# Optimization experiments

Hardware: AMD Instinct MI355X
Metric: run time of the kernel (lower is better)

The kernel has to match this reference:

```python
import jax, jax.numpy as jnp
import numpy as np

GRID_SIZE = 5
SPLINE_ORDER = 3
GRID_RANGE = (-1.0, 1.0)


def b_splines(x, grid, spline_order=SPLINE_ORDER):
    # x: [B, in], grid: [G] with G = grid_size + 2*spline_order + 1
    x = x[..., None]                      # [B, in, 1]
    g = grid[None, None, :]               # [1, 1, G]
    bases = ((x >= g[..., :-1]) & (x < g[..., 1:])).astype(x.dtype)  # [B, in, G-1]
    for k in range(1, spline_order + 1):
        left = (x - g[..., :-(k + 1)]) / (g[..., k:-1] - g[..., :-(k + 1)]) * bases[..., :-1]
        right = (g[..., k + 1:] - x) / (g[..., k + 1:] - g[..., 1:-k]) * bases[..., 1:]
        bases = left + right
    return bases                          # [B, in, grid_size + spline_order]


def setup_inputs() -> dict:
    key = jax.random.key(0)
    k1, k2, k3, k4 = jax.random.split(key, 4)
    B, IN, OUT = 32768, 256, 256
    n_coef = GRID_SIZE + SPLINE_ORDER  # 8
    h = (GRID_RANGE[1] - GRID_RANGE[0]) / GRID_SIZE
    grid = jnp.arange(-SPLINE_ORDER, GRID_SIZE + SPLINE_ORDER + 1, dtype=jnp.float32) * h + GRID_RANGE[0]  # [12]
    x = jax.random.normal(k1, (B, IN), dtype=jnp.float32)
    base_weight = jax.random.normal(k2, (OUT, IN), dtype=jnp.float32) * np.sqrt(2.0 / IN)
    spline_weight = jax.random.normal(k3, (OUT, IN, n_coef), dtype=jnp.float32) * (0.1 / GRID_SIZE)
    spline_scaler = jax.random.normal(k4, (OUT, IN), dtype=jnp.float32) * np.sqrt(2.0 / IN)
    return {"x": x, "base_weight": base_weight, "spline_weight": spline_weight,
            "spline_scaler": spline_scaler, "grid": grid}


def reference(x, base_weight, spline_weight, spline_scaler, grid):
    B = x.shape[0]
    out_features = base_weight.shape[0]
    # base branch: silu(x) @ base_weight^T
    base_out = jnp.matmul(jax.nn.silu(x), base_weight.T)  # [B, out]
    # spline branch
    bases = b_splines(x, grid)                             # [B, in, n_coef]
    scaled_w = spline_weight * spline_scaler[..., None]    # [out, in, n_coef]
    spline_out = jnp.matmul(bases.reshape(B, -1), scaled_w.reshape(out_features, -1).T)
    return base_out + spline_out
```

## Files before the change

kernel.cpp:

```cpp
#include <hip/hip_runtime.h>
#include <hip/hip_bf16.h>
#include <stdint.h>


#define IN_F 256
#define OUT_F 256
#define KDIM 2304
#define BK 64
#define NCHUNK (KDIM / BK)
#define TBINS 512
#define WC_BYTES ((size_t)OUT_F * KDIM * 2)

#define AS1 __attribute__((address_space(1)))
#define AS3 __attribute__((address_space(3)))

typedef float f32x4 __attribute__((ext_vector_type(4)));
typedef short bf16x8 __attribute__((ext_vector_type(8)));

__device__ __forceinline__ uint32_t f2bf(float f) {
    union { float f; uint32_t u; } c; c.f = f;
    uint32_t u = c.u;
    return (u + 0x7FFFu + ((u >> 16) & 1u)) >> 16;
}

__device__ __forceinline__ float silu_f(float v) {
    return v / (1.0f + __expf(-v));
}

__global__ void build_w(const float* __restrict__ bw, const float* __restrict__ sw,
                        const float* __restrict__ ss, unsigned short* __restrict__ Wc,
                        uint64_t* __restrict__ tg) {
    const int o = blockIdx.x;
    const int i = threadIdx.x;
    Wc[o * KDIM + i] = (unsigned short)f2bf(bw[o * IN_F + i]);
    const float scal = ss[o * IN_F + i];
    const float4* swv = reinterpret_cast<const float4*>(sw + (size_t)(o * IN_F + i) * 8);
    float4 s0 = swv[0], s1 = swv[1];
    uint4 wv;
    wv.x = f2bf(s0.x * scal) | (f2bf(s0.y * scal) << 16);
    wv.y = f2bf(s0.z * scal) | (f2bf(s0.w * scal) << 16);
    wv.z = f2bf(s1.x * scal) | (f2bf(s1.y * scal) << 16);
    wv.w = f2bf(s1.z * scal) | (f2bf(s1.w * scal) << 16);
    *reinterpret_cast<uint4*>(Wc + o * KDIM + IN_F + i * 8) = wv;

    if (o == 0) {
        for (int k = i; k < TBINS; k += IN_F) {
            float t = (k + 0.5f) * (1.0f / TBINS);
            float t2 = t * t, t3 = t2 * t;
            float p3 = t3 * (1.0f / 6.0f);
            float p2 = -0.5f * t3 + 0.5f * t2 + 0.5f * t + (1.0f / 6.0f);
            float p1 = 0.5f * t3 - t2 + (2.0f / 3.0f);
            float omt = 1.0f - t;
            float p0 = omt * omt * omt * (1.0f / 6.0f);
            tg[k] = (uint64_t)f2bf(p0) | ((uint64_t)f2bf(p1) << 16) |
                    ((uint64_t)f2bf(p2) << 32) | ((uint64_t)f2bf(p3) << 48);
        }
    }
}

__launch_bounds__(512, 4)
__global__ void kan_fused(const float* __restrict__ x, const unsigned short* __restrict__ Wc,
                          const uint64_t* __restrict__ tg, float* __restrict__ out) {
    __shared__ __align__(16) unsigned short As[2][128 * 64];
    __shared__ __align__(16) unsigned short Bs[2][128 * 64];

    const int bid = blockIdx.x;
    const int row0 = (bid >> 1) * 128;
    const int col0 = (bid & 1) * 128;
    const int tid = threadIdx.x;
    const int lane = tid & 63;
    const int w = tid >> 6;
    const int wm = w >> 2;
    const int wn = w & 3;
    const int l15 = lane & 15;
    const int q = lane >> 4;

    const int sr = lane >> 3;
    const int s  = lane & 7;
    const int g  = s ^ sr;
    const int srow = w * 16 + sr;

    f32x4 acc[4][2] = {};
    float xr[2][8];
    uint64_t pk2[2];
    int j02[2];

    auto stage_b = [&](int kc, int buf) {
#pragma unroll
        for (int j = 0; j < 2; ++j) {
            const unsigned short* gp =
                Wc + (size_t)(col0 + srow + j * 8) * KDIM + kc * BK + g * 8;
            __builtin_amdgcn_global_load_lds((const AS1 void*)gp,
                                             (AS3 void*)&Bs[buf][(w * 16 + j * 8) * 64],
                                             16, 0, 0);
        }
    };
    auto load_x = [&](int kc) {
        if (kc < 4) {
#pragma unroll
            for (int j = 0; j < 2; ++j) {
                const float* xp = x + (size_t)(row0 + srow + j * 8) * IN_F + kc * 64 + g * 8;
                float4 a = *reinterpret_cast<const float4*>(xp);
                float4 b = *reinterpret_cast<const float4*>(xp + 4);
                xr[j][0] = a.x; xr[j][1] = a.y; xr[j][2] = a.z; xr[j][3] = a.w;
                xr[j][4] = b.x; xr[j][5] = b.y; xr[j][6] = b.z; xr[j][7] = b.w;
            }
        } else {
            const int i0 = (kc - 4) * 8 + g;
#pragma unroll
            for (int j = 0; j < 2; ++j) {
                float xx = x[(size_t)(row0 + srow + j * 8) * IN_F + i0];
                float u = __builtin_fmaf(xx, 2.5f, 5.5f);
                float jf = floorf(u);
                int bin = (int)((u - jf) * (float)TBINS) & (TBINS - 1);
                j02[j] = (int)jf;
                pk2[j] = tg[bin];
            }
        }
    };
    auto write_a = [&](int kc, int buf) {
        if (kc < 4) {
#pragma unroll
            for (int j = 0; j < 2; ++j) {
                uint4 wv;
                wv.x = f2bf(silu_f(xr[j][0])) | (f2bf(silu_f(xr[j][1])) << 16);
                wv.y = f2bf(silu_f(xr[j][2])) | (f2bf(silu_f(xr[j][3])) << 16);
                wv.z = f2bf(silu_f(xr[j][4])) | (f2bf(silu_f(xr[j][5])) << 16);
                wv.w = f2bf(silu_f(xr[j][6])) | (f2bf(silu_f(xr[j][7])) << 16);
                *reinterpret_cast<uint4*>(&As[buf][(srow + j * 8) * 64 + s * 8]) = wv;
            }
        } else {
#pragma unroll
            for (int j = 0; j < 2; ++j) {
                int j0 = j02[j];
                uint64_t pk = ((unsigned)j0 <= 10u) ? pk2[j] : 0ull;
                int jc = j0 < 0 ? 0 : (j0 > 10 ? 10 : j0);
                int sh = jc * 16 - 48;
                unsigned __int128 v = (unsigned __int128)pk;
                v = (sh >= 0) ? (v << sh) : (v >> (-sh));
                uint4 wv;
                wv.x = (uint32_t)v;
                wv.y = (uint32_t)(v >> 32);
                wv.z = (uint32_t)(v >> 64);
                wv.w = (uint32_t)(v >> 96);
                *reinterpret_cast<uint4*>(&As[buf][(srow + j * 8) * 64 + s * 8]) = wv;
            }
        }
    };

    stage_b(0, 0);
    load_x(0);
    write_a(0, 0);
    __syncthreads();

    for (int kc = 0; kc < NCHUNK; ++kc) {
        const int cur = kc & 1;
        const int nxt = cur ^ 1;
        if (kc + 1 < NCHUNK) {
            stage_b(kc + 1, nxt);
            load_x(kc + 1);
        }
#pragma unroll
        for (int kk = 0; kk < BK; kk += 32) {
            bf16x8 af[4], bfv[2];
            const int g0 = (kk >> 3) + q;
#pragma unroll
            for (int mt = 0; mt < 4; ++mt) {
                int r = wm * 64 + mt * 16 + l15;
                af[mt] = *reinterpret_cast<const bf16x8*>(
                    &As[cur][r * 64 + ((g0 ^ (r & 7)) << 3)]);
            }
#pragma unroll
            for (int nt = 0; nt < 2; ++nt) {
                int r = wn * 32 + nt * 16 + l15;
                bfv[nt] = *reinterpret_cast<const bf16x8*>(
                    &Bs[cur][r * 64 + ((g0 ^ (r & 7)) << 3)]);
            }
#pragma unroll
            for (int mt = 0; mt < 4; ++mt)
#pragma unroll
                for (int nt = 0; nt < 2; ++nt)
                    acc[mt][nt] = __builtin_amdgcn_mfma_f32_16x16x32_bf16(
                        af[mt], bfv[nt], acc[mt][nt], 0, 0, 0);
        }
        if (kc + 1 < NCHUNK) write_a(kc + 1, nxt);
        __syncthreads();
    }

#pragma unroll
    for (int mt = 0; mt < 4; ++mt) {
        int row = row0 + wm * 64 + mt * 16 + q * 4;
#pragma unroll
        for (int nt = 0; nt < 2; ++nt) {
            int col = col0 + wn * 32 + nt * 16 + l15;
#pragma unroll
            for (int r = 0; r < 4; ++r)
                out[(size_t)(row + r) * OUT_F + col] = acc[mt][nt][r];
        }
    }
}

extern "C" void kernel_launch(void* const* d_in, const int* in_sizes, int n_in,
                              void* d_out, int out_size, void* d_ws, size_t ws_size,
                              hipStream_t stream) {
    const float* x  = (const float*)d_in[0];
    const float* bw = (const float*)d_in[1];
    const float* sw = (const float*)d_in[2];
    const float* ss = (const float*)d_in[3];
    unsigned short* Wc = (unsigned short*)d_ws;
    uint64_t* tg = (uint64_t*)((char*)d_ws + WC_BYTES);

    build_w<<<dim3(OUT_F), dim3(IN_F), 0, stream>>>(bw, sw, ss, Wc, tg);

    const int B_ROWS = in_sizes[0] / IN_F;
    kan_fused<<<dim3(B_ROWS / 128 * 2), dim3(512), 0, stream>>>(x, Wc, tg, (float*)d_out);
}
```

Measured before the change: 144.9 us.

## Widen block tile to full output width and precompute full spline basis table

Each block now computes 128 rows by all 256 output columns with 1024 threads, using 96 KB of dynamic shared memory. As a result the SiLU and B-spline A-operand is built once per row rather than once per column half, removing that duplicated work. The packed 4-coefficient table is replaced by an 11x512 table of full 16-byte rows indexed by bin and interval, so the 128-bit shift and clamping logic disappears from the inner loop. The cost is lower occupancy flexibility (one large block per CU), a larger workspace table, and more LDS traffic for B per block.

```diff
diff --git a/kernel.cpp b/kernel.cpp
--- a/kernel.cpp
+++ b/kernel.cpp
@@ -1,5 +1,4 @@
 #include <hip/hip_runtime.h>
-#include <hip/hip_bf16.h>
 #include <stdint.h>
 
 
@@ -9,6 +8,8 @@
 #define BK 64
 #define NCHUNK (KDIM / BK)
 #define TBINS 512
+#define NTAB (11 * TBINS)
+#define NTAB_PAD (NTAB + 2)
 #define WC_BYTES ((size_t)OUT_F * KDIM * 2)
 
 #define AS1 __attribute__((address_space(1)))
@@ -29,7 +30,7 @@
 
 __global__ void build_w(const float* __restrict__ bw, const float* __restrict__ sw,
                         const float* __restrict__ ss, unsigned short* __restrict__ Wc,
-                        uint64_t* __restrict__ tg) {
+                        uint4* __restrict__ tgt) {
     const int o = blockIdx.x;
     const int i = threadIdx.x;
     Wc[o * KDIM + i] = (unsigned short)f2bf(bw[o * IN_F + i]);
@@ -44,29 +45,40 @@
     *reinterpret_cast<uint4*>(Wc + o * KDIM + IN_F + i * 8) = wv;
 
     if (o == 0) {
-        for (int k = i; k < TBINS; k += IN_F) {
-            float t = (k + 0.5f) * (1.0f / TBINS);
-            float t2 = t * t, t3 = t2 * t;
-            float p3 = t3 * (1.0f / 6.0f);
-            float p2 = -0.5f * t3 + 0.5f * t2 + 0.5f * t + (1.0f / 6.0f);
-            float p1 = 0.5f * t3 - t2 + (2.0f / 3.0f);
-            float omt = 1.0f - t;
-            float p0 = omt * omt * omt * (1.0f / 6.0f);
-            tg[k] = (uint64_t)f2bf(p0) | ((uint64_t)f2bf(p1) << 16) |
-                    ((uint64_t)f2bf(p2) << 32) | ((uint64_t)f2bf(p3) << 48);
-        }
-    }
-}
-
-__launch_bounds__(512, 4)
+        for (int e = i; e < NTAB_PAD; e += IN_F) {
+            uint32_t h[4] = {0u, 0u, 0u, 0u};
+            if (e >= 1 && e <= NTAB) {
+                const int idx = e - 1;
+                const int j0 = idx >> 9;
+                const float t = ((idx & (TBINS - 1)) + 0.5f) * (1.0f / TBINS);
+                const float t2 = t * t, t3 = t2 * t;
+                float p[4];
+                p[3] = t3 * (1.0f / 6.0f);
+                p[2] = -0.5f * t3 + 0.5f * t2 + 0.5f * t + (1.0f / 6.0f);
+                p[1] = 0.5f * t3 - t2 + (2.0f / 3.0f);
+                const float omt = 1.0f - t;
+                p[0] = omt * omt * omt * (1.0f / 6.0f);
+#pragma unroll
+                for (int m = 0; m < 4; ++m) {
+                    int c = j0 - 3 + m;
+                    if (c >= 0 && c < 8) h[c >> 1] |= f2bf(p[m]) << ((c & 1) * 16);
+                }
+            }
+            uint4 e4; e4.x = h[0]; e4.y = h[1]; e4.z = h[2]; e4.w = h[3];
+            tgt[e] = e4;
+        }
+    }
+}
+
+__launch_bounds__(1024, 4)
 __global__ void kan_fused(const float* __restrict__ x, const unsigned short* __restrict__ Wc,
-                          const uint64_t* __restrict__ tg, float* __restrict__ out) {
-    __shared__ __align__(16) unsigned short As[2][128 * 64];
-    __shared__ __align__(16) unsigned short Bs[2][128 * 64];
+                          const uint4* __restrict__ tgt, float* __restrict__ out) {
+    extern __shared__ __align__(16) unsigned short smem[];
+    unsigned short* const Asb = smem;
+    unsigned short* const Bsb = smem + 2 * 128 * 64;
 
     const int bid = blockIdx.x;
-    const int row0 = (bid >> 1) * 128;
-    const int col0 = (bid & 1) * 128;
+    const int row0 = bid * 128;
     const int tid = threadIdx.x;
     const int lane = tid & 63;
     const int w = tid >> 6;
@@ -78,74 +90,49 @@
     const int sr = lane >> 3;
     const int s  = lane & 7;
     const int g  = s ^ sr;
-    const int srow = w * 16 + sr;
-
-    f32x4 acc[4][2] = {};
-    float xr[2][8];
-    uint64_t pk2[2];
-    int j02[2];
+    const int arow = w * 8 + sr;
+    const int brow = w * 16 + sr;
+
+    f32x4 acc[2][4] = {};
+    float xr[8];
+    uint4 pk;
 
     auto stage_b = [&](int kc, int buf) {
 #pragma unroll
         for (int j = 0; j < 2; ++j) {
             const unsigned short* gp =
-                Wc + (size_t)(col0 + srow + j * 8) * KDIM + kc * BK + g * 8;
+                Wc + (size_t)(brow + j * 8) * KDIM + kc * BK + g * 8;
             __builtin_amdgcn_global_load_lds((const AS1 void*)gp,
-                                             (AS3 void*)&Bs[buf][(w * 16 + j * 8) * 64],
-                                             16, 0, 0);
+                (AS3 void*)(Bsb + buf * (256 * 64) + (w * 16 + j * 8) * 64), 16, 0, 0);
         }
     };
     auto load_x = [&](int kc) {
         if (kc < 4) {
-#pragma unroll
-            for (int j = 0; j < 2; ++j) {
-                const float* xp = x + (size_t)(row0 + srow + j * 8) * IN_F + kc * 64 + g * 8;
-                float4 a = *reinterpret_cast<const float4*>(xp);
-                float4 b = *reinterpret_cast<const float4*>(xp + 4);
-                xr[j][0] = a.x; xr[j][1] = a.y; xr[j][2] = a.z; xr[j][3] = a.w;
-                xr[j][4] = b.x; xr[j][5] = b.y; xr[j][6] = b.z; xr[j][7] = b.w;
-            }
+            const float* xp = x + (size_t)(row0 + arow) * IN_F + kc * 64 + g * 8;
+            float4 a = *reinterpret_cast<const float4*>(xp);
+            float4 b = *reinterpret_cast<const float4*>(xp + 4);
+            xr[0] = a.x; xr[1] = a.y; xr[2] = a.z; xr[3] = a.w;
+            xr[4] = b.x; xr[5] = b.y; xr[6] = b.z; xr[7] = b.w;
         } else {
             const int i0 = (kc - 4) * 8 + g;
-#pragma unroll
-            for (int j = 0; j < 2; ++j) {
-                float xx = x[(size_t)(row0 + srow + j * 8) * IN_F + i0];
-                float u = __builtin_fmaf(xx, 2.5f, 5.5f);
-                float jf = floorf(u);
-                int bin = (int)((u - jf) * (float)TBINS) & (TBINS - 1);
-                j02[j] = (int)jf;
-                pk2[j] = tg[bin];
-            }
+            float xx = x[(size_t)(row0 + arow) * IN_F + i0];
+            float u = __builtin_fmaf(xx, 2.5f, 5.5f);
+            int ic = (int)floorf(u * (float)TBINS);
+            ic = ic < -1 ? -1 : (ic > NTAB ? NTAB : ic);
+            pk = tgt[ic + 1];
         }
     };
     auto write_a = [&](int kc, int buf) {
+        uint4 wv;
         if (kc < 4) {
-#pragma unroll
-            for (int j = 0; j < 2; ++j) {
-                uint4 wv;
-                wv.x = f2bf(silu_f(xr[j][0])) | (f2bf(silu_f(xr[j][1])) << 16);
-                wv.y = f2bf(silu_f(xr[j][2])) | (f2bf(silu_f(xr[j][3])) << 16);
-                wv.z = f2bf(silu_f(xr[j][4])) | (f2bf(silu_f(xr[j][5])) << 16);
-                wv.w = f2bf(silu_f(xr[j][6])) | (f2bf(silu_f(xr[j][7])) << 16);
-                *reinterpret_cast<uint4*>(&As[buf][(srow + j * 8) * 64 + s * 8]) = wv;
-            }
+            wv.x = f2bf(silu_f(xr[0])) | (f2bf(silu_f(xr[1])) << 16);
+            wv.y = f2bf(silu_f(xr[2])) | (f2bf(silu_f(xr[3])) << 16);
+            wv.z = f2bf(silu_f(xr[4])) | (f2bf(silu_f(xr[5])) << 16);
+            wv.w = f2bf(silu_f(xr[6])) | (f2bf(silu_f(xr[7])) << 16);
         } else {
-#pragma unroll
-            for (int j = 0; j < 2; ++j) {
-                int j0 = j02[j];
-                uint64_t pk = ((unsigned)j0 <= 10u) ? pk2[j] : 0ull;
-                int jc = j0 < 0 ? 0 : (j0 > 10 ? 10 : j0);
-                int sh = jc * 16 - 48;
-                unsigned __int128 v = (unsigned __int128)pk;
-                v = (sh >= 0) ? (v << sh) : (v >> (-sh));
-                uint4 wv;
-                wv.x = (uint32_t)v;
-                wv.y = (uint32_t)(v >> 32);
-                wv.z = (uint32_t)(v >> 64);
-                wv.w = (uint32_t)(v >> 96);
-                *reinterpret_cast<uint4*>(&As[buf][(srow + j * 8) * 64 + s * 8]) = wv;
-            }
-        }
+            wv = pk;
+        }
+        *reinterpret_cast<uint4*>(Asb + buf * (128 * 64) + arow * 64 + s * 8) = wv;
     };
 
     stage_b(0, 0);
@@ -160,26 +147,28 @@
             stage_b(kc + 1, nxt);
             load_x(kc + 1);
         }
+        const unsigned short* Ac = Asb + cur * (128 * 64);
+        const unsigned short* Bc = Bsb + cur * (256 * 64);
 #pragma unroll
         for (int kk = 0; kk < BK; kk += 32) {
-            bf16x8 af[4], bfv[2];
+            bf16x8 af[2], bfv[4];
             const int g0 = (kk >> 3) + q;
 #pragma unroll
-            for (int mt = 0; mt < 4; ++mt) {
-                int r = wm * 64 + mt * 16 + l15;
+            for (int mt = 0; mt < 2; ++mt) {
+                int r = wm * 32 + mt * 16 + l15;
                 af[mt] = *reinterpret_cast<const bf16x8*>(
-                    &As[cur][r * 64 + ((g0 ^ (r & 7)) << 3)]);
+                    Ac + r * 64 + ((g0 ^ (r & 7)) << 3));
             }
 #pragma unroll
-            for (int nt = 0; nt < 2; ++nt) {
-                int r = wn * 32 + nt * 16 + l15;
+            for (int nt = 0; nt < 4; ++nt) {
+                int r = wn * 64 + nt * 16 + l15;
                 bfv[nt] = *reinterpret_cast<const bf16x8*>(
-                    &Bs[cur][r * 64 + ((g0 ^ (r & 7)) << 3)]);
+                    Bc + r * 64 + ((g0 ^ (r & 7)) << 3));
             }
 #pragma unroll
-            for (int mt = 0; mt < 4; ++mt)
-#pragma unroll
-                for (int nt = 0; nt < 2; ++nt)
+            for (int mt = 0; mt < 2; ++mt)
+#pragma unroll
+                for (int nt = 0; nt < 4; ++nt)
                     acc[mt][nt] = __builtin_amdgcn_mfma_f32_16x16x32_bf16(
                         af[mt], bfv[nt], acc[mt][nt], 0, 0, 0);
         }
@@ -188,11 +177,11 @@
     }
 
 #pragma unroll
-    for (int mt = 0; mt < 4; ++mt) {
-        int row = row0 + wm * 64 + mt * 16 + q * 4;
-#pragma unroll
-        for (int nt = 0; nt < 2; ++nt) {
-            int col = col0 + wn * 32 + nt * 16 + l15;
+    for (int mt = 0; mt < 2; ++mt) {
+        int row = row0 + wm * 32 + mt * 16 + q * 4;
+#pragma unroll
+        for (int nt = 0; nt < 4; ++nt) {
+            int col = wn * 64 + nt * 16 + l15;
 #pragma unroll
             for (int r = 0; r < 4; ++r)
                 out[(size_t)(row + r) * OUT_F + col] = acc[mt][nt][r];
@@ -208,10 +197,19 @@
     const float* sw = (const float*)d_in[2];
     const float* ss = (const float*)d_in[3];
     unsigned short* Wc = (unsigned short*)d_ws;
-    uint64_t* tg = (uint64_t*)((char*)d_ws + WC_BYTES);
-
-    build_w<<<dim3(OUT_F), dim3(IN_F), 0, stream>>>(bw, sw, ss, Wc, tg);
+    uint4* tgt = (uint4*)((char*)d_ws + WC_BYTES);
+
+    static bool attr_set = false;
+    if (!attr_set) {
+        (void)hipFuncSetAttribute(reinterpret_cast<const void*>(kan_fused),
+                                  hipFuncAttributeMaxDynamicSharedMemorySize,
+                                  96 * 1024);
+        attr_set = true;
+    }
+
+    build_w<<<dim3(OUT_F), dim3(IN_F), 0, stream>>>(bw, sw, ss, Wc, tgt);
 
     const int B_ROWS = in_sizes[0] / IN_F;
-    kan_fused<<<dim3(B_ROWS / 128 * 2), dim3(512), 0, stream>>>(x, Wc, tg, (float*)d_out);
-}
+    kan_fused<<<dim3(B_ROWS / 128), dim3(1024), 96 * 1024, stream>>>(
+        x, Wc, tgt, (float*)d_out);
+}
```

Measured after the change: 146.7 us. Within noise of the previous version (+1.2%).
